# Optimization experiments

Measured on AMD Instinct MI355X. Metric: run time of the kernel, lower is better.

## Reference

```python
import jax, jax.numpy as jnp
import numpy as np

N_QUERIES = 32
N_KEYS = 128
INF = 1e10


def setup_inputs() -> dict:
    key = jax.random.key(0)
    kq, kk, kv = jax.random.split(key, 3)
    shape = (1, 16, 16384, 64)  # [B, H, N, d]
    return {
        "q": jax.random.normal(kq, shape, dtype=jnp.float32),
        "k": jax.random.normal(kk, shape, dtype=jnp.float32),
        "v": jax.random.normal(kv, shape, dtype=jnp.float32),
    }


def _local_attention(q, k, v, n_queries=N_QUERIES, n_keys=N_KEYS, inf=INF):
    # Faithful to torch _local_attention -> rearrange_to_dense_trunk -> _attention
    # (note: _attention applies NO 1/sqrt(d) scaling; we match that).
    n, d = q.shape[-2:]
    n_trunks = -(-n // n_queries)
    q_pad = n_trunks * n_queries - n
    pad_left = (n_keys - n_queries) // 2
    pad_right = int((n_trunks - 0.5) * n_queries + n_keys / 2 - n + 0.5)

    batch_dims = q.shape[:-2]
    # q -> [..., T, n_queries, d]
    qp = jnp.pad(q, [(0, 0)] * (q.ndim - 2) + [(0, q_pad), (0, 0)])
    q_t = qp.reshape(*batch_dims, n_trunks, n_queries, d)

    # k/v -> sliding windows [..., T, n_keys, d]; window t covers padded
    # positions [t*n_queries, t*n_queries + n_keys) (== torch unfold).
    win_idx = jnp.arange(n_trunks)[:, None] * n_queries + jnp.arange(n_keys)[None, :]

    def window(x):
        xp = jnp.pad(x, [(0, 0)] * (x.ndim - 2) + [(pad_left, pad_right), (0, 0)])
        return xp[..., win_idx, :]  # [..., T, n_keys, d]

    k_t = window(k)
    v_t = window(v)

    # Mask bias equivalent to the -inf padded attn_bias built in
    # rearrange_to_dense_trunk (attn_bias=None branch).
    t = jnp.arange(n_trunks)[:, None, None]
    qi = jnp.arange(n_queries)[None, :, None]
    kj = jnp.arange(n_keys)[None, None, :]
    key_pos = t * n_queries + kj - pad_left   # global key index
    row_pos = t * n_queries + qi              # global query index
    valid = (key_pos >= 0) & (key_pos < n) & (row_pos < n)
    bias = jnp.where(valid, jnp.zeros((), q.dtype), jnp.asarray(-inf, q.dtype))

    # blocked attention
    w = jnp.einsum('...tqd,...tkd->...tqk', q_t, k_t) + bias
    a = jax.nn.softmax(w, axis=-1)
    o = jnp.einsum('...tqk,...tkd->...tqd', a, v_t)

    o = o.reshape(*batch_dims, n_trunks * n_queries, d)
    return o[..., :n, :]


def reference(q, k, v):
    return _local_attention(q, k, v)
```

## Files before the change

kernel.cpp:

```cpp
#include <hip/hip_runtime.h>
#include <hip/hip_bf16.h>


typedef _Float16 f16x8 __attribute__((ext_vector_type(8)));
typedef _Float16 f16x4 __attribute__((ext_vector_type(4)));
typedef float f32x16 __attribute__((ext_vector_type(16)));
typedef unsigned int u32;
typedef u32 u32x4 __attribute__((ext_vector_type(4)));

#define NSEQ   16384
#define DHEAD  64
#define LOG2E  1.44269504088896340736f
#define TRB    4
#define BQ     (TRB * 32)
#define WROWS  (BQ + 96)
#define RSTR   128
#define KBYTES (WROWS * RSTR)

__device__ __forceinline__ int swz(int r) {
  return ((r & 7) << 4) | ((r & 8) << 3);
}

__device__ __forceinline__ u32 pk2(float a, float b) {
  auto h2 = __builtin_amdgcn_cvt_pkrtz(a, b);
  return __builtin_bit_cast(u32, h2);
}

__device__ __forceinline__ void plswap(u32& a, u32& b) {
#if __has_builtin(__builtin_amdgcn_permlane32_swap)
  typedef u32 u32x2 __attribute__((ext_vector_type(2)));
  u32x2 r = __builtin_amdgcn_permlane32_swap(a, b, false, false);
  a = r[0]; b = r[1];
#else
  const int hi = (threadIdx.x & 63) >> 5;
  u32 sa = (u32)__shfl_xor((int)a, 32);
  u32 sb = (u32)__shfl_xor((int)b, 32);
  u32 na = hi ? sb : a;
  u32 nb = hi ? b : sa;
  a = na; b = nb;
#endif
}

__device__ __forceinline__ void tr4(u32 va, f16x4& t0, f16x4& t1, f16x4& t2, f16x4& t3) {
  asm volatile("ds_read_b64_tr_b16 %0, %4 offset:0\n\t"
               "ds_read_b64_tr_b16 %1, %4 offset:1024\n\t"
               "ds_read_b64_tr_b16 %2, %4 offset:512\n\t"
               "ds_read_b64_tr_b16 %3, %4 offset:1536\n\t"
               "s_waitcnt lgkmcnt(0)"
               : "=&v"(t0), "=&v"(t1), "=&v"(t2), "=&v"(t3)
               : "v"(va));
  __builtin_amdgcn_sched_barrier(0);
}

__device__ __forceinline__ void stageK(const float* __restrict__ src, int grow0,
                                       char* __restrict__ dst, int tid) {
  const int rsub = tid >> 3;
  const int c8   = (tid & 7) * 8;
  #pragma unroll
  for (int it = 0; it < 7; ++it) {
    const int r = it * 32 + rsub;
    const int g = min(max(grow0 + r, 0), NSEQ - 1);
    const float* p = src + (size_t)g * DHEAD + c8;
    const float4 a = *reinterpret_cast<const float4*>(p);
    const float4 b = *reinterpret_cast<const float4*>(p + 4);
    const u32x4 w = {pk2(a.x, a.y), pk2(a.z, a.w), pk2(b.x, b.y), pk2(b.z, b.w)};
    *reinterpret_cast<u32x4*>(dst + ((r * RSTR + c8 * 2) ^ swz(r))) = w;
  }
}

__device__ __forceinline__ void stageV(const float* __restrict__ src, int grow0,
                                       char* __restrict__ dst, int tid) {
  const int rsub = tid >> 3;
  const int c8   = (tid & 7) * 8;
  const int dh   = c8 >> 4;
  #pragma unroll
  for (int it = 0; it < 7; ++it) {
    const int r = it * 32 + rsub;
    const int g = min(max(grow0 + r, 0), NSEQ - 1);
    const float* p = src + (size_t)g * DHEAD + c8;
    const float4 a = *reinterpret_cast<const float4*>(p);
    const float4 b = *reinterpret_cast<const float4*>(p + 4);
    const u32x4 w = {pk2(a.x, a.y), pk2(a.z, a.w), pk2(b.x, b.y), pk2(b.z, b.w)};
    const int idx = ((r >> 2) & 1) * 8 + (dh >> 1) * 4 + ((r >> 3) & 1) * 2 + (dh & 1);
    const int addr = (r >> 4) * 2048 + idx * 128 + (r & 3) * 32 + (c8 & 15) * 2;
    *reinterpret_cast<u32x4*>(dst + addr) = w;
  }
}

__global__ __launch_bounds__(256, 2) void local_attn_kernel(
    const float* __restrict__ q, const float* __restrict__ k,
    const float* __restrict__ v, float* __restrict__ out) {
  __shared__ __align__(128) char smem[2 * KBYTES];
  char* const Kc = smem;
  char* const Vc = smem + KBYTES;

  const int tid  = threadIdx.x;
  const int wave = tid >> 6;
  const int lane = tid & 63;
  const int l31  = lane & 31;
  const int hi   = lane >> 5;

  int bid = blockIdx.x;
  bid = (bid & 7) * 256 + (bid >> 3);
  const int h   = bid >> 7;
  const int q0b = (bid & 127) << 7;
  const int kg0 = q0b - 48;
  const int q0  = q0b + wave * 32;
  const int kvb = wave * 32;

  const float* __restrict__ qh = q + (size_t)h * NSEQ * DHEAD;
  const float* __restrict__ kh = k + (size_t)h * NSEQ * DHEAD;
  const float* __restrict__ vh = v + (size_t)h * NSEQ * DHEAD;

  float4 qr[4][2];
  #pragma unroll
  for (int ks = 0; ks < 4; ++ks) {
    const float* p = qh + (size_t)(q0 + l31) * DHEAD + ks * 16 + hi * 8;
    qr[ks][0] = *reinterpret_cast<const float4*>(p);
    qr[ks][1] = *reinterpret_cast<const float4*>(p + 4);
  }

  stageK(kh, kg0, Kc, tid);
  stageV(vh, kg0, Vc, tid);
  __syncthreads();

  f32x16 sacc[4] = {};
  #pragma unroll
  for (int ks = 0; ks < 4; ++ks) {
    f16x8 qf;
    qf[0] = (_Float16)(qr[ks][0].x * LOG2E); qf[1] = (_Float16)(qr[ks][0].y * LOG2E);
    qf[2] = (_Float16)(qr[ks][0].z * LOG2E); qf[3] = (_Float16)(qr[ks][0].w * LOG2E);
    qf[4] = (_Float16)(qr[ks][1].x * LOG2E); qf[5] = (_Float16)(qr[ks][1].y * LOG2E);
    qf[6] = (_Float16)(qr[ks][1].z * LOG2E); qf[7] = (_Float16)(qr[ks][1].w * LOG2E);
    #pragma unroll
    for (int kt = 0; kt < 4; ++kt) {
      const int row = kvb + kt * 32 + l31;
      const f16x8 kf = *reinterpret_cast<const f16x8*>(
          Kc + ((row * RSTR + (ks * 16 + hi * 8) * 2) ^ swz(row)));
      sacc[kt] = __builtin_amdgcn_mfma_f32_32x32x16_f16(kf, qf, sacc[kt], 0, 0, 0);
    }
  }

  if (q0 < 48 || q0 > NSEQ - 80) {
    #pragma unroll
    for (int kt = 0; kt < 4; ++kt)
      #pragma unroll
      for (int r = 0; r < 16; ++r) {
        const int key = (q0 - 48) + kt * 32 + (r & 3) + 8 * (r >> 2) + 4 * hi;
        if ((unsigned)key >= (unsigned)NSEQ) sacc[kt][r] = -1e30f;
      }
  }

  float mx = -1e30f;
  #pragma unroll
  for (int kt = 0; kt < 4; ++kt)
    #pragma unroll
    for (int r = 0; r < 16; ++r) mx = fmaxf(mx, sacc[kt][r]);
  mx = fmaxf(mx, __shfl_xor(mx, 32));
  float sum = 0.f;
  #pragma unroll
  for (int kt = 0; kt < 4; ++kt)
    #pragma unroll
    for (int r = 0; r < 16; ++r) {
      const float p = exp2f(sacc[kt][r] - mx);
      sacc[kt][r] = p;
      sum += p;
    }
  sum += __shfl_xor(sum, 32);
  const float inv = 1.0f / sum;

  f16x8 pa[4][2];
  #pragma unroll
  for (int kt = 0; kt < 4; ++kt) {
    u32 pk[8];
    #pragma unroll
    for (int c = 0; c < 8; ++c)
      pk[c] = pk2(sacc[kt][2 * c] * inv, sacc[kt][2 * c + 1] * inv);
    plswap(pk[0], pk[2]); plswap(pk[1], pk[3]);
    plswap(pk[4], pk[6]); plswap(pk[5], pk[7]);
    union { f16x8 f; u32 u[4]; } f0, f1;
    f0.u[0] = pk[0]; f0.u[1] = pk[1]; f0.u[2] = pk[2]; f0.u[3] = pk[3];
    f1.u[0] = pk[4]; f1.u[1] = pk[5]; f1.u[2] = pk[6]; f1.u[3] = pk[7];
    pa[kt][0] = f0.f;
    pa[kt][1] = f1.f;
  }

  const u32 vb = (u32)(size_t)Vc + (u32)(lane * 8);
  f32x16 oacc[2] = {};
  #pragma unroll
  for (int kt = 0; kt < 4; ++kt) {
    #pragma unroll
    for (int b = 0; b < 2; ++b) {
      const u32 va = vb + (u32)((2 * (wave + kt) + b) * 2048);
      f16x4 t0, t1, t2, t3;
      tr4(va, t0, t1, t2, t3);
      union { f16x8 f; f16x4 h[2]; } b0, b1;
      b0.h[0] = t0; b0.h[1] = t1;
      b1.h[0] = t2; b1.h[1] = t3;
      oacc[0] = __builtin_amdgcn_mfma_f32_32x32x16_f16(pa[kt][b], b0.f, oacc[0], 0, 0, 0);
      oacc[1] = __builtin_amdgcn_mfma_f32_32x32x16_f16(pa[kt][b], b1.f, oacc[1], 0, 0, 0);
    }
  }

  float* __restrict__ oh = out + (size_t)h * NSEQ * DHEAD;
  #pragma unroll
  for (int r = 0; r < 16; ++r) {
    const int row = q0 + (r & 3) + 8 * (r >> 2) + 4 * hi;
    float* po = oh + (size_t)row * DHEAD + l31;
    po[0]  = oacc[0][r];
    po[32] = oacc[1][r];
  }
}

extern "C" void kernel_launch(void* const* d_in, const int* in_sizes, int n_in,
                              void* d_out, int out_size, void* d_ws, size_t ws_size,
                              hipStream_t stream) {
  const float* q = (const float*)d_in[0];
  const float* k = (const float*)d_in[1];
  const float* v = (const float*)d_in[2];
  float* out = (float*)d_out;
  dim3 grid(2048), block(256);
  hipLaunchKernelGGL(local_attn_kernel, grid, block, 0, stream, q, k, v, out);
}
```

Before: 44.38 us.

## Load K directly from global into registers, drop K shared-memory staging

K is no longer staged through LDS. Each wave now loads its own 128 key rows straight from global memory into registers and converts them to f16 just before the QK MFMAs. This halves LDS use, so launch bounds are raised to 3 blocks per CU, and the V transposed reads are batched eight per wait instead of four. The cost is redundant global K reads across overlapping wave windows, since each key row is fetched by up to four waves instead of once per block, plus higher register pressure.

```diff
diff --git a/kernel.cpp b/kernel.cpp
--- a/kernel.cpp
+++ b/kernel.cpp
@@ -14,12 +14,7 @@
 #define TRB    4
 #define BQ     (TRB * 32)
 #define WROWS  (BQ + 96)
-#define RSTR   128
-#define KBYTES (WROWS * RSTR)
-
-__device__ __forceinline__ int swz(int r) {
-  return ((r & 7) << 4) | ((r & 8) << 3);
-}
+#define VBYTES (WROWS * 128)
 
 __device__ __forceinline__ u32 pk2(float a, float b) {
   auto h2 = __builtin_amdgcn_cvt_pkrtz(a, b);
@@ -41,31 +36,20 @@
 #endif
 }
 
-__device__ __forceinline__ void tr4(u32 va, f16x4& t0, f16x4& t1, f16x4& t2, f16x4& t3) {
-  asm volatile("ds_read_b64_tr_b16 %0, %4 offset:0\n\t"
-               "ds_read_b64_tr_b16 %1, %4 offset:1024\n\t"
-               "ds_read_b64_tr_b16 %2, %4 offset:512\n\t"
-               "ds_read_b64_tr_b16 %3, %4 offset:1536\n\t"
+__device__ __forceinline__ void tr8(u32 va, f16x4 (&t)[8]) {
+  asm volatile("ds_read_b64_tr_b16 %0, %8 offset:0\n\t"
+               "ds_read_b64_tr_b16 %1, %8 offset:1024\n\t"
+               "ds_read_b64_tr_b16 %2, %8 offset:512\n\t"
+               "ds_read_b64_tr_b16 %3, %8 offset:1536\n\t"
+               "ds_read_b64_tr_b16 %4, %8 offset:2048\n\t"
+               "ds_read_b64_tr_b16 %5, %8 offset:3072\n\t"
+               "ds_read_b64_tr_b16 %6, %8 offset:2560\n\t"
+               "ds_read_b64_tr_b16 %7, %8 offset:3584\n\t"
                "s_waitcnt lgkmcnt(0)"
-               : "=&v"(t0), "=&v"(t1), "=&v"(t2), "=&v"(t3)
+               : "=&v"(t[0]), "=&v"(t[1]), "=&v"(t[2]), "=&v"(t[3]),
+                 "=&v"(t[4]), "=&v"(t[5]), "=&v"(t[6]), "=&v"(t[7])
                : "v"(va));
   __builtin_amdgcn_sched_barrier(0);
-}
-
-__device__ __forceinline__ void stageK(const float* __restrict__ src, int grow0,
-                                       char* __restrict__ dst, int tid) {
-  const int rsub = tid >> 3;
-  const int c8   = (tid & 7) * 8;
-  #pragma unroll
-  for (int it = 0; it < 7; ++it) {
-    const int r = it * 32 + rsub;
-    const int g = min(max(grow0 + r, 0), NSEQ - 1);
-    const float* p = src + (size_t)g * DHEAD + c8;
-    const float4 a = *reinterpret_cast<const float4*>(p);
-    const float4 b = *reinterpret_cast<const float4*>(p + 4);
-    const u32x4 w = {pk2(a.x, a.y), pk2(a.z, a.w), pk2(b.x, b.y), pk2(b.z, b.w)};
-    *reinterpret_cast<u32x4*>(dst + ((r * RSTR + c8 * 2) ^ swz(r))) = w;
-  }
 }
 
 __device__ __forceinline__ void stageV(const float* __restrict__ src, int grow0,
@@ -87,12 +71,10 @@
   }
 }
 
-__global__ __launch_bounds__(256, 2) void local_attn_kernel(
+__global__ __launch_bounds__(256, 3) void local_attn_kernel(
     const float* __restrict__ q, const float* __restrict__ k,
     const float* __restrict__ v, float* __restrict__ out) {
-  __shared__ __align__(128) char smem[2 * KBYTES];
-  char* const Kc = smem;
-  char* const Vc = smem + KBYTES;
+  __shared__ __align__(128) char Vc[VBYTES];
 
   const int tid  = threadIdx.x;
   const int wave = tid >> 6;
@@ -106,7 +88,7 @@
   const int q0b = (bid & 127) << 7;
   const int kg0 = q0b - 48;
   const int q0  = q0b + wave * 32;
-  const int kvb = wave * 32;
+  const int kb0 = q0 - 48;
 
   const float* __restrict__ qh = q + (size_t)h * NSEQ * DHEAD;
   const float* __restrict__ kh = k + (size_t)h * NSEQ * DHEAD;
@@ -120,24 +102,38 @@
     qr[ks][1] = *reinterpret_cast<const float4*>(p + 4);
   }
 
-  stageK(kh, kg0, Kc, tid);
   stageV(vh, kg0, Vc, tid);
+
+  f16x8 qf[4];
+  #pragma unroll
+  for (int ks = 0; ks < 4; ++ks) {
+    qf[ks][0] = (_Float16)(qr[ks][0].x * LOG2E); qf[ks][1] = (_Float16)(qr[ks][0].y * LOG2E);
+    qf[ks][2] = (_Float16)(qr[ks][0].z * LOG2E); qf[ks][3] = (_Float16)(qr[ks][0].w * LOG2E);
+    qf[ks][4] = (_Float16)(qr[ks][1].x * LOG2E); qf[ks][5] = (_Float16)(qr[ks][1].y * LOG2E);
+    qf[ks][6] = (_Float16)(qr[ks][1].z * LOG2E); qf[ks][7] = (_Float16)(qr[ks][1].w * LOG2E);
+  }
+
   __syncthreads();
 
   f32x16 sacc[4] = {};
   #pragma unroll
-  for (int ks = 0; ks < 4; ++ks) {
-    f16x8 qf;
-    qf[0] = (_Float16)(qr[ks][0].x * LOG2E); qf[1] = (_Float16)(qr[ks][0].y * LOG2E);
-    qf[2] = (_Float16)(qr[ks][0].z * LOG2E); qf[3] = (_Float16)(qr[ks][0].w * LOG2E);
-    qf[4] = (_Float16)(qr[ks][1].x * LOG2E); qf[5] = (_Float16)(qr[ks][1].y * LOG2E);
-    qf[6] = (_Float16)(qr[ks][1].z * LOG2E); qf[7] = (_Float16)(qr[ks][1].w * LOG2E);
-    #pragma unroll
-    for (int kt = 0; kt < 4; ++kt) {
-      const int row = kvb + kt * 32 + l31;
-      const f16x8 kf = *reinterpret_cast<const f16x8*>(
-          Kc + ((row * RSTR + (ks * 16 + hi * 8) * 2) ^ swz(row)));
-      sacc[kt] = __builtin_amdgcn_mfma_f32_32x32x16_f16(kf, qf, sacc[kt], 0, 0, 0);
+  for (int kt = 0; kt < 4; ++kt) {
+    const int krow = min(max(kb0 + kt * 32 + l31, 0), NSEQ - 1);
+    const float* kp = kh + (size_t)krow * DHEAD + hi * 8;
+    float4 kr[4][2];
+    #pragma unroll
+    for (int ks = 0; ks < 4; ++ks) {
+      kr[ks][0] = *reinterpret_cast<const float4*>(kp + ks * 16);
+      kr[ks][1] = *reinterpret_cast<const float4*>(kp + ks * 16 + 4);
+    }
+    #pragma unroll
+    for (int ks = 0; ks < 4; ++ks) {
+      union { f16x8 f; u32 u[4]; } kf;
+      kf.u[0] = pk2(kr[ks][0].x, kr[ks][0].y);
+      kf.u[1] = pk2(kr[ks][0].z, kr[ks][0].w);
+      kf.u[2] = pk2(kr[ks][1].x, kr[ks][1].y);
+      kf.u[3] = pk2(kr[ks][1].z, kr[ks][1].w);
+      sacc[kt] = __builtin_amdgcn_mfma_f32_32x32x16_f16(kf.f, qf[ks], sacc[kt], 0, 0, 0);
     }
   }
 
@@ -146,7 +142,7 @@
     for (int kt = 0; kt < 4; ++kt)
       #pragma unroll
       for (int r = 0; r < 16; ++r) {
-        const int key = (q0 - 48) + kt * 32 + (r & 3) + 8 * (r >> 2) + 4 * hi;
+        const int key = kb0 + kt * 32 + (r & 3) + 8 * (r >> 2) + 4 * hi;
         if ((unsigned)key >= (unsigned)NSEQ) sacc[kt][r] = -1e30f;
       }
   }
@@ -185,21 +181,21 @@
     pa[kt][1] = f1.f;
   }
 
-  const u32 vb = (u32)(size_t)Vc + (u32)(lane * 8);
+  const u32 vb = (u32)(size_t)(&Vc[0]) + (u32)(lane * 8);
   f32x16 oacc[2] = {};
   #pragma unroll
   for (int kt = 0; kt < 4; ++kt) {
-    #pragma unroll
-    for (int b = 0; b < 2; ++b) {
-      const u32 va = vb + (u32)((2 * (wave + kt) + b) * 2048);
-      f16x4 t0, t1, t2, t3;
-      tr4(va, t0, t1, t2, t3);
-      union { f16x8 f; f16x4 h[2]; } b0, b1;
-      b0.h[0] = t0; b0.h[1] = t1;
-      b1.h[0] = t2; b1.h[1] = t3;
-      oacc[0] = __builtin_amdgcn_mfma_f32_32x32x16_f16(pa[kt][b], b0.f, oacc[0], 0, 0, 0);
-      oacc[1] = __builtin_amdgcn_mfma_f32_32x32x16_f16(pa[kt][b], b1.f, oacc[1], 0, 0, 0);
-    }
+    f16x4 t[8];
+    tr8(vb + (u32)(2 * (wave + kt) * 2048), t);
+    union { f16x8 f; f16x4 h[2]; } b00, b01, b10, b11;
+    b00.h[0] = t[0]; b00.h[1] = t[1];
+    b01.h[0] = t[2]; b01.h[1] = t[3];
+    b10.h[0] = t[4]; b10.h[1] = t[5];
+    b11.h[0] = t[6]; b11.h[1] = t[7];
+    oacc[0] = __builtin_amdgcn_mfma_f32_32x32x16_f16(pa[kt][0], b00.f, oacc[0], 0, 0, 0);
+    oacc[1] = __builtin_amdgcn_mfma_f32_32x32x16_f16(pa[kt][0], b01.f, oacc[1], 0, 0, 0);
+    oacc[0] = __builtin_amdgcn_mfma_f32_32x32x16_f16(pa[kt][1], b10.f, oacc[0], 0, 0, 0);
+    oacc[1] = __builtin_amdgcn_mfma_f32_32x32x16_f16(pa[kt][1], b11.f, oacc[1], 0, 0, 0);
   }
 
   float* __restrict__ oh = out + (size_t)h * NSEQ * DHEAD;
```

New measurement: 59.31 us. 33.7% more time.
